# Kernel optimization log

Hardware: AMD Instinct MI355X
Metric: run time of the kernel (lower is better)

The kernel has to match this reference:

```python
import jax, jax.numpy as jnp
import numpy as np

N_NODES = 1_000_000
N_EDGES = 4_000_000  # knn_k = 4
N_GRAPHS = 1024
HIDDEN = 64
N_FEAT = 4


def setup_inputs() -> dict:
    key = jax.random.key(0)
    k0, k1, k2, k3, k4 = jax.random.split(key, 5)
    x = jax.random.normal(k0, (N_NODES, N_FEAT), dtype=jnp.float32)
    edge_index = jax.random.randint(k1, (2, N_EDGES), 0, N_NODES, dtype=jnp.int64)
    batch = jnp.sort(jax.random.randint(k2, (N_NODES,), 0, N_GRAPHS, dtype=jnp.int64))
    W1 = jax.random.normal(k3, (N_FEAT, HIDDEN), dtype=jnp.float32) * 0.5
    b1 = jnp.zeros((HIDDEN,), dtype=jnp.float32)
    W2 = jax.random.normal(k4, (HIDDEN, 1), dtype=jnp.float32) * 0.1
    b2 = jnp.zeros((1,), dtype=jnp.float32)
    return {"x": x, "W1": W1, "b1": b1, "W2": W2, "b2": b2,
            "edge_index": edge_index, "batch": batch}


def gcn_conv(x, edge_index, W, b):
    # PyG GCNConv: linear transform, add self-loops, sym-normalize, scatter-add.
    n = x.shape[0]
    h = x @ W  # [N, 64]
    loop = jnp.arange(n, dtype=edge_index.dtype)
    row = jnp.concatenate([edge_index[0], loop])  # source j
    col = jnp.concatenate([edge_index[1], loop])  # target i
    deg = jax.ops.segment_sum(jnp.ones_like(col, dtype=h.dtype), col, num_segments=n)
    dis = jnp.where(deg > 0, jax.lax.rsqrt(jnp.maximum(deg, 1.0)), 0.0)
    norm = dis[row] * dis[col]  # [E+N]
    out = jax.ops.segment_sum(h[row] * norm[:, None], col, num_segments=n)
    return out + b


def reference(x, W1, b1, W2, b2, edge_index, batch):
    h = gcn_conv(x, edge_index, W1, b1)          # [N, 64]
    h = jax.nn.elu(h)                            # ELU activation
    pooled = jax.ops.segment_sum(h, batch, num_segments=N_GRAPHS)  # global_add_pool
    return pooled @ W2 + b2                      # [G, 1]
```

## Files before the change

### kernel.cpp

```cpp
#include <hip/hip_runtime.h>
#include <hip/hip_fp16.h>

#define N_NODES 1000000
#define N_EDGES 4000000
#define N_GRAPHS 1024
#define HIDDEN 64

#define G1 1000
#define T1 512
#define EPB (N_EDGES / G1)
#define EPB4 (EPB / 4)
#define BSHIFT 11
#define BSIZE 2048
#define NBK 512
#define NBUCK ((N_NODES + BSIZE - 1) / BSIZE)

typedef int      vi4 __attribute__((ext_vector_type(4)));
typedef unsigned vu4 __attribute__((ext_vector_type(4)));

__device__ __forceinline__ int4 nt_int4(const int4* p) {
    vi4 v = __builtin_nontemporal_load((const vi4*)p);
    return make_int4(v.x, v.y, v.z, v.w);
}
__device__ __forceinline__ uint4 nt_uint4(const uint4* p) {
    vu4 v = __builtin_nontemporal_load((const vu4*)p);
    return make_uint4(v.x, v.y, v.z, v.w);
}

__global__ __launch_bounds__(T1) void k_hist(const int4* __restrict__ col4,
                                             int* __restrict__ part,
                                             float* __restrict__ out,
                                             const float* __restrict__ b2) {
    __shared__ int h[NBK];
    int t = threadIdx.x, blk = blockIdx.x;
    for (int i = t; i < NBK; i += T1) h[i] = 0;
    int gid = blk * T1 + t;
    if (gid < N_GRAPHS) out[gid] = b2[0];
    __syncthreads();
    int b0 = blk * EPB4;
    for (int i = t; i < EPB4; i += T1) {
        int4 c = nt_int4(col4 + b0 + i);
        atomicAdd(&h[((unsigned)c.x) >> BSHIFT], 1);
        atomicAdd(&h[((unsigned)c.y) >> BSHIFT], 1);
        atomicAdd(&h[((unsigned)c.z) >> BSHIFT], 1);
        atomicAdd(&h[((unsigned)c.w) >> BSHIFT], 1);
    }
    __syncthreads();
    for (int i = t; i < NBK; i += T1) part[blk * NBK + i] = h[i];
}

__global__ __launch_bounds__(1024) void k_colscan(int* __restrict__ part,
                                                  int* __restrict__ ecnt) {
    int b = blockIdx.x;
    int t = threadIdx.x;
    __shared__ int a[1024];
    int v = (t < G1) ? part[t * NBK + b] : 0;
    a[t] = v;
    __syncthreads();
    for (int o = 1; o < 1024; o <<= 1) {
        int u = (t >= o) ? a[t - o] : 0;
        __syncthreads();
        a[t] += u;
        __syncthreads();
    }
    if (t < G1) part[t * NBK + b] = a[t] - v;
    if (t == 1023) ecnt[b] = a[1023];
}

__global__ __launch_bounds__(NBK) void k_bscan(const int* __restrict__ ecnt,
                                               int* __restrict__ ebase) {
    __shared__ int sc[NBK];
    int b = threadIdx.x;
    int run4 = (ecnt[b] + 3) & ~3;
    sc[b] = run4;
    __syncthreads();
    for (int o = 1; o < NBK; o <<= 1) {
        int v = (b >= o) ? sc[b - o] : 0;
        __syncthreads();
        sc[b] += v;
        __syncthreads();
    }
    ebase[b] = sc[b] - run4;
}

__global__ __launch_bounds__(T1) void k_part(const int4* __restrict__ row4,
                                             const int4* __restrict__ col4,
                                             const int* __restrict__ part,
                                             const int* __restrict__ ebase,
                                             unsigned* __restrict__ epair) {
    __shared__ int cur[NBK];
    int t = threadIdx.x, blk = blockIdx.x;
    for (int i = t; i < NBK; i += T1) cur[i] = part[blk * NBK + i] + ebase[i];
    __syncthreads();
    int b0 = blk * EPB4;
    for (int i = t; i < EPB4; i += T1) {
        int4 c = nt_int4(col4 + b0 + i);
        int4 r = nt_int4(row4 + b0 + i);
        int cc[4] = {c.x, c.y, c.z, c.w};
        int rr[4] = {r.x, r.y, r.z, r.w};
        #pragma unroll
        for (int k = 0; k < 4; ++k) {
            int b = ((unsigned)cc[k]) >> BSHIFT;
            int pos = atomicAdd(&cur[b], 1);
            epair[pos] = ((unsigned)(cc[k] & (BSIZE - 1)) << 20) | (unsigned)rr[k];
        }
    }
}

__global__ __launch_bounds__(1024) void k_deg2(const unsigned* __restrict__ epair,
                                               const int* __restrict__ ebase,
                                               const int* __restrict__ ecnt,
                                               const float4* __restrict__ x,
                                               float* __restrict__ dis,
                                               uint2* __restrict__ xdh) {
    __shared__ int deg[BSIZE];
    int t = threadIdx.x, b = blockIdx.x;
    for (int i = t; i < BSIZE; i += 1024) deg[i] = 1;
    __syncthreads();
    int ne = ecnt[b];
    const unsigned* ep = epair + ebase[b];
    int ne4 = ne & ~3;
    for (int i = 4 * t; i < ne4; i += 4096) {
        uint4 u = nt_uint4((const uint4*)(ep + i));
        atomicAdd(&deg[u.x >> 20], 1);
        atomicAdd(&deg[u.y >> 20], 1);
        atomicAdd(&deg[u.z >> 20], 1);
        atomicAdd(&deg[u.w >> 20], 1);
    }
    for (int i = ne4 + t; i < ne; i += 1024) atomicAdd(&deg[ep[i] >> 20], 1);
    __syncthreads();
    int n0 = b << BSHIFT;
    for (int i = t; i < BSIZE; i += 1024) {
        int node = n0 + i;
        if (node < N_NODES) {
            float d = rsqrtf((float)deg[i]);
            dis[node] = d;
            float4 xv = x[node];
            __half2 h01 = __floats2half2_rn(xv.x * d, xv.y * d);
            __half2 h23 = __floats2half2_rn(xv.z * d, xv.w * d);
            uint2 pk;
            pk.x = *(unsigned*)&h01;
            pk.y = *(unsigned*)&h23;
            xdh[node] = pk;
        }
    }
}

__device__ __forceinline__ void acc_edge(unsigned u, uint2 p, float* sf) {
    int loc = u >> 20;
    __half2 h01 = *(__half2*)&p.x;
    __half2 h23 = *(__half2*)&p.y;
    float2 f01 = __half22float2(h01);
    float2 f23 = __half22float2(h23);
    float* sp = sf + loc * 5;
    atomicAdd(sp + 0, f01.x);
    atomicAdd(sp + 1, f01.y);
    atomicAdd(sp + 2, f23.x);
    atomicAdd(sp + 3, f23.y);
}

__global__ __launch_bounds__(1024) void k_acc(const unsigned* __restrict__ epair,
                                              const int* __restrict__ ebase,
                                              const int* __restrict__ ecnt,
                                              const uint2* __restrict__ xdh,
                                              float4* __restrict__ sbuf) {
    __shared__ float sf[BSIZE * 5];
    int t = threadIdx.x, b = blockIdx.x;
    for (int i = t; i < BSIZE * 5; i += 1024) sf[i] = 0.f;
    __syncthreads();
    int ne = ecnt[b];
    const unsigned* ep = epair + ebase[b];
    int ne4 = ne & ~3;
    for (int i = 4 * t; i < ne4; i += 4096) {
        unsigned u0 = ep[i], u1 = ep[i + 1], u2 = ep[i + 2], u3 = ep[i + 3];
        uint2 p0 = xdh[u0 & 0xFFFFFu];
        uint2 p1 = xdh[u1 & 0xFFFFFu];
        uint2 p2 = xdh[u2 & 0xFFFFFu];
        uint2 p3 = xdh[u3 & 0xFFFFFu];
        acc_edge(u0, p0, sf);
        acc_edge(u1, p1, sf);
        acc_edge(u2, p2, sf);
        acc_edge(u3, p3, sf);
    }
    for (int i = ne4 + t; i < ne; i += 1024) {
        unsigned u = ep[i];
        acc_edge(u, xdh[u & 0xFFFFFu], sf);
    }
    __syncthreads();
    int n0 = b << BSHIFT;
    for (int i = t; i < BSIZE; i += 1024) {
        int node = n0 + i;
        if (node < N_NODES) {
            const float* q = sf + i * 5;
            sbuf[node] = make_float4(q[0], q[1], q[2], q[3]);
        }
    }
}

__global__ __launch_bounds__(256) void k_mlp(const float4* __restrict__ sbuf,
                                             const uint2* __restrict__ xdh,
                                             const float* __restrict__ dis,
                                             const int* __restrict__ batch,
                                             const float* __restrict__ W1,
                                             const float* __restrict__ b1,
                                             const float* __restrict__ W2,
                                             float* __restrict__ out) {
    int n = blockIdx.x * blockDim.x + threadIdx.x;
    bool valid = n < N_NODES;
    float acc = 0.f;
    int g = -1;
    if (valid) {
        float4 sv = sbuf[n];
        uint2 p = xdh[n];
        __half2 h01 = *(__half2*)&p.x;
        __half2 h23 = *(__half2*)&p.y;
        float2 f01 = __half22float2(h01);
        float2 f23 = __half22float2(h23);
        float d = dis[n];
        float u0 = d * (sv.x + f01.x);
        float u1 = d * (sv.y + f01.y);
        float u2 = d * (sv.z + f23.x);
        float u3 = d * (sv.w + f23.y);
        g = batch[n];
        #pragma unroll
        for (int k = 0; k < HIDDEN; ++k) {
            float t = fmaf(u0, W1[k],
                      fmaf(u1, W1[HIDDEN + k],
                      fmaf(u2, W1[2 * HIDDEN + k],
                      fmaf(u3, W1[3 * HIDDEN + k], b1[k]))));
            float h = t > 0.f ? t : (__expf(t) - 1.f);
            acc = fmaf(h, W2[k], acc);
        }
    }
    unsigned long long rem = __ballot(valid);
    while (rem) {
        int leader = __ffsll(rem) - 1;
        int gl = __shfl(g, leader);
        bool mine = valid && (g == gl);
        unsigned long long mask = __ballot(mine);
        float v = mine ? acc : 0.f;
        #pragma unroll
        for (int o = 32; o; o >>= 1) v += __shfl_xor(v, o);
        if ((int)(threadIdx.x & 63) == leader) unsafeAtomicAdd(&out[gl], v);
        rem &= ~mask;
    }
}

__global__ __launch_bounds__(256) void k_init(int* __restrict__ deg, float4* __restrict__ s,
                                              float* __restrict__ out, const float* __restrict__ b2) {
    int i = blockIdx.x * blockDim.x + threadIdx.x;
    if (i < N_NODES) { deg[i] = 1; s[i] = make_float4(0.f, 0.f, 0.f, 0.f); }
    if (i < N_GRAPHS) out[i] = b2[0];
}
__global__ __launch_bounds__(256) void k_deg(const int* __restrict__ col, int* __restrict__ deg) {
    int e = blockIdx.x * blockDim.x + threadIdx.x;
    if (e < N_EDGES) atomicAdd(&deg[col[e]], 1);
}
__global__ __launch_bounds__(256) void k_dis(const int* __restrict__ deg, float* __restrict__ dis) {
    int i = blockIdx.x * blockDim.x + threadIdx.x;
    if (i < N_NODES) dis[i] = rsqrtf((float)deg[i]);
}
__global__ __launch_bounds__(256) void k_scatter(const int* __restrict__ row, const int* __restrict__ col,
                                                 const float4* __restrict__ x, const float* __restrict__ dis,
                                                 float* __restrict__ s) {
    int e = blockIdx.x * blockDim.x + threadIdx.x;
    if (e >= N_EDGES) return;
    int j = row[e], i = col[e];
    float dj = dis[j];
    float4 xj = x[j];
    float* sp = s + 4ll * (long long)i;
    unsafeAtomicAdd(sp + 0, xj.x * dj);
    unsafeAtomicAdd(sp + 1, xj.y * dj);
    unsafeAtomicAdd(sp + 2, xj.z * dj);
    unsafeAtomicAdd(sp + 3, xj.w * dj);
}
__global__ __launch_bounds__(256) void k_node(const float4* __restrict__ x, const float4* __restrict__ s,
                                              const float* __restrict__ dis, const int* __restrict__ batch,
                                              const float* __restrict__ W1, const float* __restrict__ b1,
                                              const float* __restrict__ W2, float* __restrict__ out) {
    int n = blockIdx.x * blockDim.x + threadIdx.x;
    bool valid = n < N_NODES;
    float acc = 0.f; int g = -1;
    if (valid) {
        float4 xn = x[n], sn = s[n];
        float di = dis[n], inv = di * di;
        float u0 = di * sn.x + inv * xn.x, u1 = di * sn.y + inv * xn.y;
        float u2 = di * sn.z + inv * xn.z, u3 = di * sn.w + inv * xn.w;
        g = batch[n];
        #pragma unroll
        for (int k = 0; k < HIDDEN; ++k) {
            float t = fmaf(u0, W1[k], fmaf(u1, W1[HIDDEN + k],
                      fmaf(u2, W1[2 * HIDDEN + k], fmaf(u3, W1[3 * HIDDEN + k], b1[k]))));
            float h = t > 0.f ? t : expm1f(t);
            acc = fmaf(h, W2[k], acc);
        }
    }
    unsigned long long rem = __ballot(valid);
    while (rem) {
        int leader = __ffsll(rem) - 1;
        int gl = __shfl(g, leader);
        bool mine = valid && (g == gl);
        unsigned long long mask = __ballot(mine);
        float v = mine ? acc : 0.f;
        #pragma unroll
        for (int o = 32; o; o >>= 1) v += __shfl_xor(v, o);
        if ((int)(threadIdx.x & 63) == leader) unsafeAtomicAdd(&out[gl], v);
        rem &= ~mask;
    }
}

extern "C" void kernel_launch(void* const* d_in, const int* in_sizes, int n_in,
                              void* d_out, int out_size, void* d_ws, size_t ws_size,
                              hipStream_t stream) {
    const float* x   = (const float*)d_in[0];
    const float* W1  = (const float*)d_in[1];
    const float* b1  = (const float*)d_in[2];
    const float* W2  = (const float*)d_in[3];
    const float* b2  = (const float*)d_in[4];
    const int*   ei  = (const int*)d_in[5];
    const int*   bat = (const int*)d_in[6];
    float* out = (float*)d_out;

    const int* row = ei;
    const int* col = ei + N_EDGES;
    char* ws = (char*)d_ws;

    size_t o_ep   = 0;
    size_t o_sb   = o_ep + (size_t)(N_EDGES + 4 * NBK) * 4;
    size_t o_xdh  = o_sb + (size_t)N_NODES * 16;
    size_t o_dis  = o_xdh + (size_t)N_NODES * 8;
    size_t o_part = o_dis + (size_t)N_NODES * 4;
    size_t o_eb   = o_part + (size_t)G1 * NBK * 4;
    size_t o_ec   = o_eb + NBK * 4;
    size_t need   = o_ec + NBK * 4;

    if (ws_size >= need) {
        unsigned* epair = (unsigned*)(ws + o_ep);
        float4*   sbuf  = (float4*)(ws + o_sb);
        uint2*    xdh   = (uint2*)(ws + o_xdh);
        float*    dis   = (float*)(ws + o_dis);
        int*      part  = (int*)(ws + o_part);
        int*      ebase = (int*)(ws + o_eb);
        int*      ecnt  = (int*)(ws + o_ec);

        k_hist<<<G1, T1, 0, stream>>>((const int4*)col, part, out, b2);
        k_colscan<<<NBK, 1024, 0, stream>>>(part, ecnt);
        k_bscan<<<1, NBK, 0, stream>>>(ecnt, ebase);
        k_part<<<G1, T1, 0, stream>>>((const int4*)row, (const int4*)col, part, ebase, epair);
        k_deg2<<<NBUCK, 1024, 0, stream>>>(epair, ebase, ecnt, (const float4*)x, dis, xdh);
        k_acc<<<NBUCK, 1024, 0, stream>>>(epair, ebase, ecnt, xdh, sbuf);
        k_mlp<<<(N_NODES + 255) / 256, 256, 0, stream>>>(sbuf, xdh, dis, bat, W1, b1, W2, out);
    } else {
        int nb_n = (N_NODES + 255) / 256;
        int nb_e = (N_EDGES + 255) / 256;
        int*    deg = (int*)(ws);
        float*  dis = (float*)(ws + (size_t)N_NODES * 4);
        float*  s   = (float*)(ws + (size_t)N_NODES * 8);
        float4* s4  = (float4*)s;
        k_init<<<nb_n, 256, 0, stream>>>(deg, s4, out, b2);
        k_deg<<<nb_e, 256, 0, stream>>>(col, deg);
        k_dis<<<nb_n, 256, 0, stream>>>(deg, dis);
        k_scatter<<<nb_e, 256, 0, stream>>>(row, col, (const float4*)x, dis, s);
        k_node<<<nb_n, 256, 0, stream>>>((const float4*)x, s4, dis, bat, W1, b1, W2, out);
    }
}
```

Baseline: 193.5 us.

## Shrink partition grid to 250 blocks and store aggregated sums as fp16

```diff
diff --git a/kernel.cpp b/kernel.cpp
--- a/kernel.cpp
+++ b/kernel.cpp
@@ -6,7 +6,7 @@
 #define N_GRAPHS 1024
 #define HIDDEN 64
 
-#define G1 1000
+#define G1 250
 #define T1 512
 #define EPB (N_EDGES / G1)
 #define EPB4 (EPB / 4)
@@ -49,22 +49,22 @@
     for (int i = t; i < NBK; i += T1) part[blk * NBK + i] = h[i];
 }
 
-__global__ __launch_bounds__(1024) void k_colscan(int* __restrict__ part,
-                                                  int* __restrict__ ecnt) {
+__global__ __launch_bounds__(256) void k_colscan(int* __restrict__ part,
+                                                 int* __restrict__ ecnt) {
     int b = blockIdx.x;
     int t = threadIdx.x;
-    __shared__ int a[1024];
+    __shared__ int a[256];
     int v = (t < G1) ? part[t * NBK + b] : 0;
     a[t] = v;
     __syncthreads();
-    for (int o = 1; o < 1024; o <<= 1) {
+    for (int o = 1; o < 256; o <<= 1) {
         int u = (t >= o) ? a[t - o] : 0;
         __syncthreads();
         a[t] += u;
         __syncthreads();
     }
     if (t < G1) part[t * NBK + b] = a[t] - v;
-    if (t == 1023) ecnt[b] = a[1023];
+    if (t == 255) ecnt[b] = a[255];
 }
 
 __global__ __launch_bounds__(NBK) void k_bscan(const int* __restrict__ ecnt,
@@ -163,7 +163,7 @@
                                               const int* __restrict__ ebase,
                                               const int* __restrict__ ecnt,
                                               const uint2* __restrict__ xdh,
-                                              float4* __restrict__ sbuf) {
+                                              uint2* __restrict__ sbuf) {
     __shared__ float sf[BSIZE * 5];
     int t = threadIdx.x, b = blockIdx.x;
     for (int i = t; i < BSIZE * 5; i += 1024) sf[i] = 0.f;
@@ -192,12 +192,17 @@
         int node = n0 + i;
         if (node < N_NODES) {
             const float* q = sf + i * 5;
-            sbuf[node] = make_float4(q[0], q[1], q[2], q[3]);
-        }
-    }
-}
-
-__global__ __launch_bounds__(256) void k_mlp(const float4* __restrict__ sbuf,
+            __half2 s01 = __floats2half2_rn(q[0], q[1]);
+            __half2 s23 = __floats2half2_rn(q[2], q[3]);
+            uint2 pk;
+            pk.x = *(unsigned*)&s01;
+            pk.y = *(unsigned*)&s23;
+            sbuf[node] = pk;
+        }
+    }
+}
+
+__global__ __launch_bounds__(256) void k_mlp(const uint2* __restrict__ sbuf,
                                              const uint2* __restrict__ xdh,
                                              const float* __restrict__ dis,
                                              const int* __restrict__ batch,
@@ -210,17 +215,17 @@
     float acc = 0.f;
     int g = -1;
     if (valid) {
-        float4 sv = sbuf[n];
+        uint2 sv = sbuf[n];
         uint2 p = xdh[n];
-        __half2 h01 = *(__half2*)&p.x;
-        __half2 h23 = *(__half2*)&p.y;
-        float2 f01 = __half22float2(h01);
-        float2 f23 = __half22float2(h23);
+        float2 s01 = __half22float2(*(__half2*)&sv.x);
+        float2 s23 = __half22float2(*(__half2*)&sv.y);
+        float2 f01 = __half22float2(*(__half2*)&p.x);
+        float2 f23 = __half22float2(*(__half2*)&p.y);
         float d = dis[n];
-        float u0 = d * (sv.x + f01.x);
-        float u1 = d * (sv.y + f01.y);
-        float u2 = d * (sv.z + f23.x);
-        float u3 = d * (sv.w + f23.y);
+        float u0 = d * (s01.x + f01.x);
+        float u1 = d * (s01.y + f01.y);
+        float u2 = d * (s23.x + f23.x);
+        float u3 = d * (s23.y + f23.y);
         g = batch[n];
         #pragma unroll
         for (int k = 0; k < HIDDEN; ++k) {
@@ -327,7 +332,7 @@
 
     size_t o_ep   = 0;
     size_t o_sb   = o_ep + (size_t)(N_EDGES + 4 * NBK) * 4;
-    size_t o_xdh  = o_sb + (size_t)N_NODES * 16;
+    size_t o_xdh  = o_sb + (size_t)N_NODES * 8;
     size_t o_dis  = o_xdh + (size_t)N_NODES * 8;
     size_t o_part = o_dis + (size_t)N_NODES * 4;
     size_t o_eb   = o_part + (size_t)G1 * NBK * 4;
@@ -336,7 +341,7 @@
 
     if (ws_size >= need) {
         unsigned* epair = (unsigned*)(ws + o_ep);
-        float4*   sbuf  = (float4*)(ws + o_sb);
+        uint2*    sbuf  = (uint2*)(ws + o_sb);
         uint2*    xdh   = (uint2*)(ws + o_xdh);
         float*    dis   = (float*)(ws + o_dis);
         int*      part  = (int*)(ws + o_part);
@@ -344,7 +349,7 @@
         int*      ecnt  = (int*)(ws + o_ec);
 
         k_hist<<<G1, T1, 0, stream>>>((const int4*)col, part, out, b2);
-        k_colscan<<<NBK, 1024, 0, stream>>>(part, ecnt);
+        k_colscan<<<NBK, 256, 0, stream>>>(part, ecnt);
         k_bscan<<<1, NBK, 0, stream>>>(ecnt, ebase);
         k_part<<<G1, T1, 0, stream>>>((const int4*)row, (const int4*)col, part, ebase, epair);
         k_deg2<<<NBUCK, 1024, 0, stream>>>(epair, ebase, ecnt, (const float4*)x, dis, xdh);
```

New measurement: 183.4 us. -5.2%, faster.
